# Optimization experiments

Hardware: AMD Instinct MI355X
Metric: run time of the kernel (lower is better)

The kernel has to match this reference:

```python
import jax, jax.numpy as jnp
import numpy as np

N, E, M, D = 100000, 50000, 1000000, 128  # vertices, hyperedges, incidences, hidden


def setup_inputs() -> dict:
    key = jax.random.key(0)
    ks = jax.random.split(key, 9)
    v = jax.random.normal(ks[0], (N, D), dtype=jnp.float32)
    e = jax.random.normal(ks[1], (E, D), dtype=jnp.float32)
    vidx = jax.random.randint(ks[2], (M,), 0, N)
    eidx = jax.random.randint(ks[3], (M,), 0, E)
    v_reg_weight = jax.random.uniform(ks[4], (M, 1), dtype=jnp.float32)
    e_reg_weight = jax.random.uniform(ks[5], (M, 1), dtype=jnp.float32)
    v_reg_sum = jnp.ones((N, 1), dtype=jnp.float32)
    e_reg_sum = jnp.ones((E, 1), dtype=jnp.float32)
    # learned parameters
    W_v2e = jax.random.normal(ks[6], (D, D), dtype=jnp.float32)
    W_e2v = jax.random.normal(ks[7], (D, D), dtype=jnp.float32)
    b_v = jnp.zeros((D,), dtype=jnp.float32)
    b_e = jnp.zeros((D,), dtype=jnp.float32)
    v_weight = jax.random.uniform(ks[8], (N, 1), dtype=jnp.float32)  # args.v_weight
    return dict(v=v, e=e, vidx=vidx, eidx=eidx,
                v_reg_weight=v_reg_weight, e_reg_weight=e_reg_weight,
                v_reg_sum=v_reg_sum, e_reg_sum=e_reg_sum,
                W_v2e=W_v2e, W_e2v=W_e2v, b_v=b_v, b_e=b_e, v_weight=v_weight)


def reference(v, e, vidx, eidx, v_reg_weight, e_reg_weight, v_reg_sum, e_reg_sum,
              W_v2e, W_e2v, b_v, b_e, v_weight):
    # v2e: dense transform, gather by vidx, reweight, scatter_add into edges
    ve = jax.nn.relu(v @ W_v2e + b_v)                      # [N, D]
    v_out = v * v_weight * 4.0                             # v_fac = 4
    msg_ve = (ve * v_weight)[vidx] * v_reg_weight          # [M, D]
    e_out = e + jax.ops.segment_sum(msg_ve, eidx, num_segments=E)
    e_out = e_out / e_reg_sum
    # e2v: dense transform, gather by eidx, reweight, scatter_add into vertices
    ev = jax.nn.relu(e_out @ W_e2v + b_e)                  # [E, D]
    msg_ev = (ev / 3.0)[eidx] * e_reg_weight               # [M, D]
    v_out = v_out + jax.ops.segment_sum(msg_ev, vidx, num_segments=N)
    v_out = v_out / v_reg_sum
    # is_last_mod=True: no dropout
    return v_out, e_out
```

## Files before the change

kernel.cpp:

```cpp
#include <hip/hip_runtime.h>
#include <cstddef>

#define DD 128
#define PART_ELEMS 4096
#define MAXB 256
#define MAXW 512
#define WT_LD 136

typedef __attribute__((ext_vector_type(8))) short bf16x8;
typedef __attribute__((ext_vector_type(4))) float f32x4;

__device__ __forceinline__ unsigned bf16pk(float x, float y) {
    unsigned a = __float_as_uint(x);
    unsigned b = __float_as_uint(y);
    a = (a + 0x7FFFu + ((a >> 16) & 1u)) >> 16;
    b = (b + 0x7FFFu + ((b >> 16) & 1u)) >> 16;
    return a | (b << 16);
}
__device__ __forceinline__ unsigned short bf16r(float x) {
    unsigned u = __float_as_uint(x);
    return (unsigned short)((u + 0x7FFFu + ((u >> 16) & 1u)) >> 16);
}
__device__ __forceinline__ float bflo(unsigned u) { return __uint_as_float(u << 16); }
__device__ __forceinline__ float bfhi(unsigned u) { return __uint_as_float(u & 0xFFFF0000u); }

__global__ __launch_bounds__(256)
void conv_w_kernel(const float* __restrict__ W0, const float* __restrict__ W1,
                   unsigned short* __restrict__ Wt0, unsigned short* __restrict__ Wt1,
                   int* __restrict__ bcur_e, int* __restrict__ bcur_v, int e_cap, int v_cap)
{
    int idx = blockIdx.x * 256 + threadIdx.x;
    int k = idx >> 7, c = idx & 127;
    Wt0[c * 128 + k] = bf16r(W0[idx]);
    Wt1[c * 128 + k] = bf16r(W1[idx]);
    if (blockIdx.x == 0) {
        bcur_e[threadIdx.x] = threadIdx.x * e_cap;
        bcur_v[threadIdx.x] = threadIdx.x * v_cap;
    }
}

__global__ __launch_bounds__(256)
void part2_kernel(const int* __restrict__ eidx, const int* __restrict__ vidx,
                  const float* __restrict__ vrw, const float* __restrict__ erw,
                  int* __restrict__ bcur_e, int* __restrict__ bcur_v,
                  int2* __restrict__ tmp_e, int2* __restrict__ tmp_v,
                  int M, int e_shift, int v_shift, int e_bk, int v_bk)
{
    __shared__ int lcnt_e[MAXB], lbase_e[MAXB], lcnt_v[MAXB], lbase_v[MAXB];
    const int t = threadIdx.x;
    const int base = blockIdx.x * PART_ELEMS;
    const int end = min(base + PART_ELEMS, M);

    if (t < e_bk) lcnt_e[t] = 0;
    if (t < v_bk) lcnt_v[t] = 0;
    __syncthreads();
    for (int j = base + t; j < end; j += 256) {
        atomicAdd(&lcnt_e[eidx[j] >> e_shift], 1);
        atomicAdd(&lcnt_v[vidx[j] >> v_shift], 1);
    }
    __syncthreads();
    if (t < e_bk) { int c = lcnt_e[t]; lbase_e[t] = c ? atomicAdd(&bcur_e[t], c) : 0; lcnt_e[t] = 0; }
    if (t < v_bk) { int c = lcnt_v[t]; lbase_v[t] = c ? atomicAdd(&bcur_v[t], c) : 0; lcnt_v[t] = 0; }
    __syncthreads();
    for (int j = base + t; j < end; j += 256) {
        int ei = eidx[j], vi = vidx[j];
        int wqe = (int)(vrw[j] * 32767.0f + 0.5f); wqe = wqe < 32767 ? wqe : 32767;
        int wqv = (int)(erw[j] * 32767.0f + 0.5f); wqv = wqv < 32767 ? wqv : 32767;
        int be = ei >> e_shift;
        int pe = lbase_e[be] + atomicAdd(&lcnt_e[be], 1);
        tmp_e[pe] = make_int2(ei | (wqe << 17), vi);
        int bv = vi >> v_shift;
        int pv = lbase_v[bv] + atomicAdd(&lcnt_v[bv], 1);
        tmp_v[pv] = make_int2(vi | (wqv << 17), ei);
    }
}

struct FineLds { int lcnt[MAXW]; int lstart[MAXW]; int sdata[256]; int scnt[256]; int spbase; };
struct GemmLds { unsigned short Wt[128 * WT_LD]; unsigned short At[64 * WT_LD]; };

__device__ __forceinline__
void fine_body(int blk, FineLds& L,
               const int2* __restrict__ tmp_e, const int* __restrict__ bcur_e,
               int e_cap, int e_shift, int En, int e_bk,
               int* __restrict__ e_start, unsigned* __restrict__ e_pack,
               const int2* __restrict__ tmp_v, const int* __restrict__ bcur_v,
               int v_cap, int v_shift, int Nn, int v_bk,
               int* __restrict__ v_start, unsigned* __restrict__ v_pack, int M)
{
    const int t = threadIdx.x;
    const int2* tmp; const int* bcur; int cap, shift, n, nb, b;
    int* start; unsigned* pack;
    if (blk < e_bk) {
        tmp = tmp_e; bcur = bcur_e; cap = e_cap; shift = e_shift; n = En; nb = e_bk;
        start = e_start; pack = e_pack; b = blk;
    } else {
        tmp = tmp_v; bcur = bcur_v; cap = v_cap; shift = v_shift; n = Nn; nb = v_bk;
        start = v_start; pack = v_pack; b = blk - e_bk;
    }

    int cnt_t = (t < nb) ? (bcur[t] - t * cap) : 0;
    L.scnt[t] = cnt_t;
    __syncthreads();
    int xx = cnt_t;
    for (int off = 1; off < 256; off <<= 1) {
        int y = (t >= off) ? L.scnt[t - off] : 0;
        __syncthreads();
        xx += y;
        L.scnt[t] = xx;
        __syncthreads();
    }
    if (t == b) L.spbase = xx - cnt_t;
    if (b == nb - 1 && t == 0) start[n] = M;
    __syncthreads();
    const int pbase = L.spbase;

    const int d0 = b << shift;
    const int width = min(1 << shift, n - d0);
    const int tbase = b * cap;
    const int nrec = bcur[b] - tbase;

    L.lcnt[t] = 0; L.lcnt[t + 256] = 0;
    __syncthreads();
    for (int j = t; j < nrec; j += 256)
        atomicAdd(&L.lcnt[(tmp[tbase + j].x & 0x1FFFF) - d0], 1);
    __syncthreads();
    int a = L.lcnt[2 * t], bb = L.lcnt[2 * t + 1];
    int s = a + bb;
    L.sdata[t] = s;
    __syncthreads();
    int x = s;
    for (int off = 1; off < 256; off <<= 1) {
        int y = (t >= off) ? L.sdata[t - off] : 0;
        __syncthreads();
        x += y;
        L.sdata[t] = x;
        __syncthreads();
    }
    int ex = x - s;
    L.lstart[2 * t] = ex;
    L.lstart[2 * t + 1] = ex + a;
    L.lcnt[2 * t] = 0; L.lcnt[2 * t + 1] = 0;
    __syncthreads();
    for (int i = t; i < width; i += 256)
        start[d0 + i] = pbase + L.lstart[i];
    for (int j = t; j < nrec; j += 256) {
        int2 r = tmp[tbase + j];
        int di = (r.x & 0x1FFFF) - d0;
        int pos = pbase + L.lstart[di] + atomicAdd(&L.lcnt[di], 1);
        pack[pos] = (unsigned)r.y | (((unsigned)r.x >> 17) << 17);
    }
}

__device__ __forceinline__
void gemm_body(int blk, GemmLds& L, const float* __restrict__ A,
               const unsigned short* __restrict__ Wtg, const float* __restrict__ bias,
               const float* __restrict__ rowwt, unsigned* __restrict__ outb,
               int nrows, float scale, bool v2e)
{
    const int t = threadIdx.x;
    const int row0 = blk * 64;

    {
        int r = t >> 1, h = t & 1;
        const uint4* src = reinterpret_cast<const uint4*>(Wtg + r * 128 + h * 64);
        uint4* dst = reinterpret_cast<uint4*>(&L.Wt[r * WT_LD + h * 64]);
        #pragma unroll
        for (int i = 0; i < 8; ++i) dst[i] = src[i];
    }
    {
        int r = t >> 2, q = t & 3;
        int grow = row0 + r;
        uint4 o[4];
        if (grow < nrows) {
            const float4* src = reinterpret_cast<const float4*>(A + (size_t)grow * DD + q * 32);
            #pragma unroll
            for (int i = 0; i < 4; ++i) {
                float4 f0 = src[2 * i];
                float4 f1 = src[2 * i + 1];
                o[i].x = bf16pk(f0.x, f0.y);
                o[i].y = bf16pk(f0.z, f0.w);
                o[i].z = bf16pk(f1.x, f1.y);
                o[i].w = bf16pk(f1.z, f1.w);
            }
        } else {
            #pragma unroll
            for (int i = 0; i < 4; ++i) o[i] = make_uint4(0, 0, 0, 0);
        }
        uint4* dst = reinterpret_cast<uint4*>(&L.At[r * WT_LD + q * 32]);
        #pragma unroll
        for (int i = 0; i < 4; ++i) dst[i] = o[i];
    }
    __syncthreads();

    const int w  = t >> 6;
    const int l  = t & 63;
    const int lr = l & 15;
    const int lk = (l >> 4) * 8;

    f32x4 acc[8];
    #pragma unroll
    for (int i = 0; i < 8; ++i) acc[i] = 0.0f;

    const int arow = w * 16 + lr;
    #pragma unroll
    for (int ks = 0; ks < 4; ++ks) {
        bf16x8 af = *reinterpret_cast<const bf16x8*>(&L.At[arow * WT_LD + lk + ks * 32]);
        #pragma unroll
        for (int ct = 0; ct < 8; ++ct) {
            bf16x8 bfr = *reinterpret_cast<const bf16x8*>(&L.Wt[(ct * 16 + lr) * WT_LD + lk + ks * 32]);
            acc[ct] = __builtin_amdgcn_mfma_f32_16x16x32_bf16(af, bfr, acc[ct], 0, 0, 0);
        }
    }

    float bcol[8];
    #pragma unroll
    for (int ct = 0; ct < 8; ++ct) bcol[ct] = bias[ct * 16 + lr];
    #pragma unroll
    for (int r = 0; r < 4; ++r) {
        int rl = w * 16 + (l >> 4) * 4 + r;
        int grow = row0 + rl;
        float rw = scale;
        if (v2e) rw = (grow < nrows) ? rowwt[grow] : 0.f;
        #pragma unroll
        for (int ct = 0; ct < 8; ++ct) {
            float val = fmaxf(acc[ct][r] + bcol[ct], 0.f) * rw;
            L.At[rl * WT_LD + ct * 16 + lr] = bf16r(val);
        }
    }
    {
        int r = t >> 2, part = t & 3;
        int grow = row0 + r;
        if (grow < nrows) {
            const uint4* src = reinterpret_cast<const uint4*>(&L.At[r * WT_LD + part * 32]);
            uint4* dst = reinterpret_cast<uint4*>(outb + (size_t)grow * 64 + part * 16);
            dst[0] = src[0]; dst[1] = src[1]; dst[2] = src[2]; dst[3] = src[3];
        }
    }
}

__global__ __launch_bounds__(256)
void fused_fine_gemm_kernel(const int2* __restrict__ tmp_e, const int* __restrict__ bcur_e,
                            int e_cap, int e_shift, int En, int e_bk,
                            int* __restrict__ e_start, unsigned* __restrict__ e_pack,
                            const int2* __restrict__ tmp_v, const int* __restrict__ bcur_v,
                            int v_cap, int v_shift, int Nn, int v_bk,
                            int* __restrict__ v_start, unsigned* __restrict__ v_pack, int M,
                            const float* __restrict__ v, const unsigned short* __restrict__ Wt0,
                            const float* __restrict__ bv, const float* __restrict__ vweight,
                            unsigned* __restrict__ vwb)
{
    __shared__ union SM { FineLds f; GemmLds g; } sm;
    const int nfine = e_bk + v_bk;
    if ((int)blockIdx.x < nfine) {
        fine_body(blockIdx.x, sm.f, tmp_e, bcur_e, e_cap, e_shift, En, e_bk, e_start, e_pack,
                  tmp_v, bcur_v, v_cap, v_shift, Nn, v_bk, v_start, v_pack, M);
    } else {
        gemm_body(blockIdx.x - nfine, sm.g, v, Wt0, bv, vweight, vwb, Nn, 1.0f, true);
    }
}

__global__ __launch_bounds__(256)
void gemm_mfma_kernel(const float* __restrict__ A, const unsigned short* __restrict__ Wtg,
                      const float* __restrict__ bias, unsigned* __restrict__ outb,
                      int nrows, float scale)
{
    __shared__ GemmLds sm;
    gemm_body(blockIdx.x, sm, A, Wtg, bias, nullptr, outb, nrows, scale, false);
}

__global__ __launch_bounds__(256)
void e_agg_kernel(const float* __restrict__ e, const unsigned* __restrict__ vwb,
                  const int* __restrict__ start, const unsigned* __restrict__ pack,
                  const float* __restrict__ ers, float* __restrict__ eout, int E)
{
    int row = blockIdx.x * 16 + (threadIdx.x >> 4);
    if (row >= E) return;
    int ql = threadIdx.x & 15;
    int s = start[row], t = start[row + 1];

    float a0=0.f,a1=0.f,a2=0.f,a3=0.f,a4=0.f,a5=0.f,a6=0.f,a7=0.f;
    float b0=0.f,b1=0.f,b2=0.f,b3=0.f,b4=0.f,b5=0.f,b6=0.f,b7=0.f;

    int j = s;
    for (; j + 2 <= t; j += 2) {
        unsigned pw0 = pack[j];
        unsigned pw1 = pack[j + 1];
        uint4 u0 = *reinterpret_cast<const uint4*>(&vwb[(size_t)(pw0 & 0x1FFFFu) * 64 + ql * 4]);
        uint4 u1 = *reinterpret_cast<const uint4*>(&vwb[(size_t)(pw1 & 0x1FFFFu) * 64 + ql * 4]);
        float w0 = (float)(pw0 >> 17) * (1.0f / 32767.0f);
        float w1 = (float)(pw1 >> 17) * (1.0f / 32767.0f);
        a0 = fmaf(bflo(u0.x), w0, a0); a1 = fmaf(bfhi(u0.x), w0, a1);
        a2 = fmaf(bflo(u0.y), w0, a2); a3 = fmaf(bfhi(u0.y), w0, a3);
        a4 = fmaf(bflo(u0.z), w0, a4); a5 = fmaf(bfhi(u0.z), w0, a5);
        a6 = fmaf(bflo(u0.w), w0, a6); a7 = fmaf(bfhi(u0.w), w0, a7);
        b0 = fmaf(bflo(u1.x), w1, b0); b1 = fmaf(bfhi(u1.x), w1, b1);
        b2 = fmaf(bflo(u1.y), w1, b2); b3 = fmaf(bfhi(u1.y), w1, b3);
        b4 = fmaf(bflo(u1.z), w1, b4); b5 = fmaf(bfhi(u1.z), w1, b5);
        b6 = fmaf(bflo(u1.w), w1, b6); b7 = fmaf(bfhi(u1.w), w1, b7);
    }
    if (j < t) {
        unsigned pw = pack[j];
        float wm = (float)(pw >> 17) * (1.0f / 32767.0f);
        uint4 u = *reinterpret_cast<const uint4*>(&vwb[(size_t)(pw & 0x1FFFFu) * 64 + ql * 4]);
        a0 = fmaf(bflo(u.x), wm, a0); a1 = fmaf(bfhi(u.x), wm, a1);
        a2 = fmaf(bflo(u.y), wm, a2); a3 = fmaf(bfhi(u.y), wm, a3);
        a4 = fmaf(bflo(u.z), wm, a4); a5 = fmaf(bfhi(u.z), wm, a5);
        a6 = fmaf(bflo(u.w), wm, a6); a7 = fmaf(bfhi(u.w), wm, a7);
    }
    float r0 = a0 + b0, r1 = a1 + b1, r2 = a2 + b2, r3 = a3 + b3;
    float r4 = a4 + b4, r5 = a5 + b5, r6 = a6 + b6, r7 = a7 + b7;

    float rs = 1.0f / ers[row];
    const float4* ep = reinterpret_cast<const float4*>(&e[(size_t)row * DD + ql * 8]);
    float4 e0 = ep[0], e1 = ep[1];
    float4 o0 = make_float4((e0.x + r0) * rs, (e0.y + r1) * rs, (e0.z + r2) * rs, (e0.w + r3) * rs);
    float4 o1 = make_float4((e1.x + r4) * rs, (e1.y + r5) * rs, (e1.z + r6) * rs, (e1.w + r7) * rs);
    float4* op = reinterpret_cast<float4*>(&eout[(size_t)row * DD + ql * 8]);
    op[0] = o0; op[1] = o1;
}

__global__ __launch_bounds__(256)
void v_agg_kernel(const float* __restrict__ v, const unsigned* __restrict__ evb,
                  const int* __restrict__ start, const unsigned* __restrict__ pack,
                  const float* __restrict__ vrs, const float* __restrict__ vweight,
                  float* __restrict__ vout, int N)
{
    int row = blockIdx.x * 16 + (threadIdx.x >> 4);
    if (row >= N) return;
    int ql = threadIdx.x & 15;
    int s = start[row], t = start[row + 1];

    float a0=0.f,a1=0.f,a2=0.f,a3=0.f,a4=0.f,a5=0.f,a6=0.f,a7=0.f;
    float b0=0.f,b1=0.f,b2=0.f,b3=0.f,b4=0.f,b5=0.f,b6=0.f,b7=0.f;

    int j = s;
    for (; j + 2 <= t; j += 2) {
        unsigned pw0 = pack[j];
        unsigned pw1 = pack[j + 1];
        uint4 u0 = *reinterpret_cast<const uint4*>(&evb[(size_t)(pw0 & 0x1FFFFu) * 64 + ql * 4]);
        uint4 u1 = *reinterpret_cast<const uint4*>(&evb[(size_t)(pw1 & 0x1FFFFu) * 64 + ql * 4]);
        float w0 = (float)(pw0 >> 17) * (1.0f / 32767.0f);
        float w1 = (float)(pw1 >> 17) * (1.0f / 32767.0f);
        a0 = fmaf(bflo(u0.x), w0, a0); a1 = fmaf(bfhi(u0.x), w0, a1);
        a2 = fmaf(bflo(u0.y), w0, a2); a3 = fmaf(bfhi(u0.y), w0, a3);
        a4 = fmaf(bflo(u0.z), w0, a4); a5 = fmaf(bfhi(u0.z), w0, a5);
        a6 = fmaf(bflo(u0.w), w0, a6); a7 = fmaf(bfhi(u0.w), w0, a7);
        b0 = fmaf(bflo(u1.x), w1, b0); b1 = fmaf(bfhi(u1.x), w1, b1);
        b2 = fmaf(bflo(u1.y), w1, b2); b3 = fmaf(bfhi(u1.y), w1, b3);
        b4 = fmaf(bflo(u1.z), w1, b4); b5 = fmaf(bfhi(u1.z), w1, b5);
        b6 = fmaf(bflo(u1.w), w1, b6); b7 = fmaf(bfhi(u1.w), w1, b7);
    }
    if (j < t) {
        unsigned pw = pack[j];
        float wm = (float)(pw >> 17) * (1.0f / 32767.0f);
        uint4 u = *reinterpret_cast<const uint4*>(&evb[(size_t)(pw & 0x1FFFFu) * 64 + ql * 4]);
        a0 = fmaf(bflo(u.x), wm, a0); a1 = fmaf(bfhi(u.x), wm, a1);
        a2 = fmaf(bflo(u.y), wm, a2); a3 = fmaf(bfhi(u.y), wm, a3);
        a4 = fmaf(bflo(u.z), wm, a4); a5 = fmaf(bfhi(u.z), wm, a5);
        a6 = fmaf(bflo(u.w), wm, a6); a7 = fmaf(bfhi(u.w), wm, a7);
    }
    float r0 = a0 + b0, r1 = a1 + b1, r2 = a2 + b2, r3 = a3 + b3;
    float r4 = a4 + b4, r5 = a5 + b5, r6 = a6 + b6, r7 = a7 + b7;

    float rs = 1.0f / vrs[row];
    float wt = vweight[row] * 4.0f;
    const float4* vp = reinterpret_cast<const float4*>(&v[(size_t)row * DD + ql * 8]);
    float4 v0 = vp[0], v1 = vp[1];
    float4 o0 = make_float4((v0.x * wt + r0) * rs, (v0.y * wt + r1) * rs,
                            (v0.z * wt + r2) * rs, (v0.w * wt + r3) * rs);
    float4 o1 = make_float4((v1.x * wt + r4) * rs, (v1.y * wt + r5) * rs,
                            (v1.z * wt + r6) * rs, (v1.w * wt + r7) * rs);
    float4* op = reinterpret_cast<float4*>(&vout[(size_t)row * DD + ql * 8]);
    op[0] = o0; op[1] = o1;
}

extern "C" void kernel_launch(void* const* d_in, const int* in_sizes, int n_in,
                              void* d_out, int out_size, void* d_ws, size_t ws_size,
                              hipStream_t stream)
{
    const float* v       = (const float*)d_in[0];
    const float* e       = (const float*)d_in[1];
    const int*   vidx    = (const int*)d_in[2];
    const int*   eidx    = (const int*)d_in[3];
    const float* vrw     = (const float*)d_in[4];
    const float* erw     = (const float*)d_in[5];
    const float* vrs     = (const float*)d_in[6];
    const float* ers     = (const float*)d_in[7];
    const float* Wv2e    = (const float*)d_in[8];
    const float* We2v    = (const float*)d_in[9];
    const float* bv      = (const float*)d_in[10];
    const float* be      = (const float*)d_in[11];
    const float* vweight = (const float*)d_in[12];

    const int N = in_sizes[0] / DD;
    const int E = in_sizes[1] / DD;
    const int M = in_sizes[2];

    float* vout = (float*)d_out;
    float* eout = vout + (size_t)N * DD;

    auto calc_shift = [](int n) {
        int s = 0;
        while (((n + (1 << s) - 1) >> s) > MAXB) ++s;
        return s;
    };
    const int e_shift = calc_shift(E);
    const int v_shift = calc_shift(N);
    const int e_bk = (E + (1 << e_shift) - 1) >> e_shift;
    const int v_bk = (N + (1 << v_shift) - 1) >> v_shift;
    const int e_cap = ((M / e_bk) * 3) / 2 + 256;
    const int v_cap = ((M / v_bk) * 3) / 2 + 256;

    char* wsb = (char*)d_ws;
    size_t off = 0;
    auto alloc = [&](size_t bytes) { char* p = wsb + off; off += (bytes + 255) & ~(size_t)255; return p; };
    unsigned* vwb   = (unsigned*)alloc((size_t)N * 64 * sizeof(unsigned));
    unsigned* evb   = vwb;
    int*   e_start = (int*)alloc((size_t)(E + 1) * sizeof(int));
    int*   v_start = (int*)alloc((size_t)(N + 1) * sizeof(int));
    int*   bcur_e  = (int*)alloc(MAXB * sizeof(int));
    int*   bcur_v  = (int*)alloc(MAXB * sizeof(int));
    unsigned short* Wt0 = (unsigned short*)alloc(DD * DD * sizeof(unsigned short));
    unsigned short* Wt1 = (unsigned short*)alloc(DD * DD * sizeof(unsigned short));
    unsigned* e_pack = (unsigned*)alloc((size_t)M * sizeof(unsigned));
    unsigned* v_pack = (unsigned*)alloc((size_t)M * sizeof(unsigned));
    int2*  tmp_e   = (int2*)alloc((size_t)e_bk * e_cap * sizeof(int2));
    int2*  tmp_v   = (int2*)alloc((size_t)v_bk * v_cap * sizeof(int2));

    const int pblk = (M + PART_ELEMS - 1) / PART_ELEMS;
    const int gblkN = (N + 63) / 64;

    conv_w_kernel<<<64, 256, 0, stream>>>(Wv2e, We2v, Wt0, Wt1, bcur_e, bcur_v, e_cap, v_cap);
    part2_kernel<<<pblk, 256, 0, stream>>>(eidx, vidx, vrw, erw, bcur_e, bcur_v,
                                           tmp_e, tmp_v, M, e_shift, v_shift, e_bk, v_bk);
    fused_fine_gemm_kernel<<<e_bk + v_bk + gblkN, 256, 0, stream>>>(
        tmp_e, bcur_e, e_cap, e_shift, E, e_bk, e_start, e_pack,
        tmp_v, bcur_v, v_cap, v_shift, N, v_bk, v_start, v_pack, M,
        v, Wt0, bv, vweight, vwb);
    e_agg_kernel<<<(E + 15) / 16, 256, 0, stream>>>(e, vwb, e_start, e_pack, ers, eout, E);
    gemm_mfma_kernel<<<(E + 63) / 64, 256, 0, stream>>>(eout, Wt1, be, evb, E, 1.0f / 3.0f);
    v_agg_kernel<<<(N + 15) / 16, 256, 0, stream>>>(v, evb, v_start, v_pack, vrs, vweight, vout, N);
}
```

Measured before the change: 187.8 us.

## Fuse edge aggregation with e2v GEMM and read weights from global memory

The edge aggregation and the e2v MFMA GEMM are merged into one kernel. Each block aggregates 64 edge rows, writes eout, packs the rows to bf16 in LDS and runs the GEMM on them directly, so eout is no longer read back from global memory and one launch is removed. The weight tile is no longer staged in LDS; B fragments are read from global memory (likely L2-resident), which cuts LDS use but adds uncoalesced global reads. Bucket cursors are now zeroed with memsets and the per-bucket offsets are applied in the partition kernel, and evb gets its own buffer instead of aliasing vwb.

```diff
diff --git a/kernel.cpp b/kernel.cpp
--- a/kernel.cpp
+++ b/kernel.cpp
@@ -26,17 +26,12 @@
 
 __global__ __launch_bounds__(256)
 void conv_w_kernel(const float* __restrict__ W0, const float* __restrict__ W1,
-                   unsigned short* __restrict__ Wt0, unsigned short* __restrict__ Wt1,
-                   int* __restrict__ bcur_e, int* __restrict__ bcur_v, int e_cap, int v_cap)
+                   unsigned short* __restrict__ Wt0, unsigned short* __restrict__ Wt1)
 {
     int idx = blockIdx.x * 256 + threadIdx.x;
     int k = idx >> 7, c = idx & 127;
     Wt0[c * 128 + k] = bf16r(W0[idx]);
     Wt1[c * 128 + k] = bf16r(W1[idx]);
-    if (blockIdx.x == 0) {
-        bcur_e[threadIdx.x] = threadIdx.x * e_cap;
-        bcur_v[threadIdx.x] = threadIdx.x * v_cap;
-    }
 }
 
 __global__ __launch_bounds__(256)
@@ -44,7 +39,8 @@
                   const float* __restrict__ vrw, const float* __restrict__ erw,
                   int* __restrict__ bcur_e, int* __restrict__ bcur_v,
                   int2* __restrict__ tmp_e, int2* __restrict__ tmp_v,
-                  int M, int e_shift, int v_shift, int e_bk, int v_bk)
+                  int M, int e_shift, int v_shift, int e_bk, int v_bk,
+                  int e_cap, int v_cap)
 {
     __shared__ int lcnt_e[MAXB], lbase_e[MAXB], lcnt_v[MAXB], lbase_v[MAXB];
     const int t = threadIdx.x;
@@ -59,8 +55,8 @@
         atomicAdd(&lcnt_v[vidx[j] >> v_shift], 1);
     }
     __syncthreads();
-    if (t < e_bk) { int c = lcnt_e[t]; lbase_e[t] = c ? atomicAdd(&bcur_e[t], c) : 0; lcnt_e[t] = 0; }
-    if (t < v_bk) { int c = lcnt_v[t]; lbase_v[t] = c ? atomicAdd(&bcur_v[t], c) : 0; lcnt_v[t] = 0; }
+    if (t < e_bk) { int c = lcnt_e[t]; lbase_e[t] = t * e_cap + (c ? atomicAdd(&bcur_e[t], c) : 0); lcnt_e[t] = 0; }
+    if (t < v_bk) { int c = lcnt_v[t]; lbase_v[t] = t * v_cap + (c ? atomicAdd(&bcur_v[t], c) : 0); lcnt_v[t] = 0; }
     __syncthreads();
     for (int j = base + t; j < end; j += 256) {
         int ei = eidx[j], vi = vidx[j];
@@ -76,7 +72,7 @@
 }
 
 struct FineLds { int lcnt[MAXW]; int lstart[MAXW]; int sdata[256]; int scnt[256]; int spbase; };
-struct GemmLds { unsigned short Wt[128 * WT_LD]; unsigned short At[64 * WT_LD]; };
+struct GemmLds { unsigned short At[64 * WT_LD]; };
 
 __device__ __forceinline__
 void fine_body(int blk, FineLds& L,
@@ -98,7 +94,7 @@
         start = v_start; pack = v_pack; b = blk - e_bk;
     }
 
-    int cnt_t = (t < nb) ? (bcur[t] - t * cap) : 0;
+    int cnt_t = (t < nb) ? bcur[t] : 0;
     L.scnt[t] = cnt_t;
     __syncthreads();
     int xx = cnt_t;
@@ -117,7 +113,7 @@
     const int d0 = b << shift;
     const int width = min(1 << shift, n - d0);
     const int tbase = b * cap;
-    const int nrec = bcur[b] - tbase;
+    const int nrec = bcur[b];
 
     L.lcnt[t] = 0; L.lcnt[t + 256] = 0;
     __syncthreads();
@@ -152,21 +148,13 @@
 }
 
 __device__ __forceinline__
-void gemm_body(int blk, GemmLds& L, const float* __restrict__ A,
-               const unsigned short* __restrict__ Wtg, const float* __restrict__ bias,
-               const float* __restrict__ rowwt, unsigned* __restrict__ outb,
-               int nrows, float scale, bool v2e)
+void gemm_body_v2e(int blk, GemmLds& L, const float* __restrict__ A,
+                   const unsigned short* __restrict__ Wtg, const float* __restrict__ bias,
+                   const float* __restrict__ rowwt, unsigned* __restrict__ outb, int nrows)
 {
     const int t = threadIdx.x;
     const int row0 = blk * 64;
 
-    {
-        int r = t >> 1, h = t & 1;
-        const uint4* src = reinterpret_cast<const uint4*>(Wtg + r * 128 + h * 64);
-        uint4* dst = reinterpret_cast<uint4*>(&L.Wt[r * WT_LD + h * 64]);
-        #pragma unroll
-        for (int i = 0; i < 8; ++i) dst[i] = src[i];
-    }
     {
         int r = t >> 2, q = t & 3;
         int grow = row0 + r;
@@ -207,7 +195,7 @@
         bf16x8 af = *reinterpret_cast<const bf16x8*>(&L.At[arow * WT_LD + lk + ks * 32]);
         #pragma unroll
         for (int ct = 0; ct < 8; ++ct) {
-            bf16x8 bfr = *reinterpret_cast<const bf16x8*>(&L.Wt[(ct * 16 + lr) * WT_LD + lk + ks * 32]);
+            bf16x8 bfr = *reinterpret_cast<const bf16x8*>(&Wtg[(ct * 16 + lr) * 128 + lk + ks * 32]);
             acc[ct] = __builtin_amdgcn_mfma_f32_16x16x32_bf16(af, bfr, acc[ct], 0, 0, 0);
         }
     }
@@ -219,8 +207,7 @@
     for (int r = 0; r < 4; ++r) {
         int rl = w * 16 + (l >> 4) * 4 + r;
         int grow = row0 + rl;
-        float rw = scale;
-        if (v2e) rw = (grow < nrows) ? rowwt[grow] : 0.f;
+        float rw = (grow < nrows) ? rowwt[grow] : 0.f;
         #pragma unroll
         for (int ct = 0; ct < 8; ++ct) {
             float val = fmaxf(acc[ct][r] + bcol[ct], 0.f) * rw;
@@ -255,68 +242,117 @@
         fine_body(blockIdx.x, sm.f, tmp_e, bcur_e, e_cap, e_shift, En, e_bk, e_start, e_pack,
                   tmp_v, bcur_v, v_cap, v_shift, Nn, v_bk, v_start, v_pack, M);
     } else {
-        gemm_body(blockIdx.x - nfine, sm.g, v, Wt0, bv, vweight, vwb, Nn, 1.0f, true);
+        gemm_body_v2e(blockIdx.x - nfine, sm.g, v, Wt0, bv, vweight, vwb, Nn);
     }
 }
 
 __global__ __launch_bounds__(256)
-void gemm_mfma_kernel(const float* __restrict__ A, const unsigned short* __restrict__ Wtg,
-                      const float* __restrict__ bias, unsigned* __restrict__ outb,
-                      int nrows, float scale)
-{
-    __shared__ GemmLds sm;
-    gemm_body(blockIdx.x, sm, A, Wtg, bias, nullptr, outb, nrows, scale, false);
-}
-
-__global__ __launch_bounds__(256)
-void e_agg_kernel(const float* __restrict__ e, const unsigned* __restrict__ vwb,
-                  const int* __restrict__ start, const unsigned* __restrict__ pack,
-                  const float* __restrict__ ers, float* __restrict__ eout, int E)
-{
-    int row = blockIdx.x * 16 + (threadIdx.x >> 4);
-    if (row >= E) return;
-    int ql = threadIdx.x & 15;
-    int s = start[row], t = start[row + 1];
-
-    float a0=0.f,a1=0.f,a2=0.f,a3=0.f,a4=0.f,a5=0.f,a6=0.f,a7=0.f;
-    float b0=0.f,b1=0.f,b2=0.f,b3=0.f,b4=0.f,b5=0.f,b6=0.f,b7=0.f;
-
-    int j = s;
-    for (; j + 2 <= t; j += 2) {
-        unsigned pw0 = pack[j];
-        unsigned pw1 = pack[j + 1];
-        uint4 u0 = *reinterpret_cast<const uint4*>(&vwb[(size_t)(pw0 & 0x1FFFFu) * 64 + ql * 4]);
-        uint4 u1 = *reinterpret_cast<const uint4*>(&vwb[(size_t)(pw1 & 0x1FFFFu) * 64 + ql * 4]);
-        float w0 = (float)(pw0 >> 17) * (1.0f / 32767.0f);
-        float w1 = (float)(pw1 >> 17) * (1.0f / 32767.0f);
-        a0 = fmaf(bflo(u0.x), w0, a0); a1 = fmaf(bfhi(u0.x), w0, a1);
-        a2 = fmaf(bflo(u0.y), w0, a2); a3 = fmaf(bfhi(u0.y), w0, a3);
-        a4 = fmaf(bflo(u0.z), w0, a4); a5 = fmaf(bfhi(u0.z), w0, a5);
-        a6 = fmaf(bflo(u0.w), w0, a6); a7 = fmaf(bfhi(u0.w), w0, a7);
-        b0 = fmaf(bflo(u1.x), w1, b0); b1 = fmaf(bfhi(u1.x), w1, b1);
-        b2 = fmaf(bflo(u1.y), w1, b2); b3 = fmaf(bfhi(u1.y), w1, b3);
-        b4 = fmaf(bflo(u1.z), w1, b4); b5 = fmaf(bfhi(u1.z), w1, b5);
-        b6 = fmaf(bflo(u1.w), w1, b6); b7 = fmaf(bfhi(u1.w), w1, b7);
-    }
-    if (j < t) {
-        unsigned pw = pack[j];
-        float wm = (float)(pw >> 17) * (1.0f / 32767.0f);
-        uint4 u = *reinterpret_cast<const uint4*>(&vwb[(size_t)(pw & 0x1FFFFu) * 64 + ql * 4]);
-        a0 = fmaf(bflo(u.x), wm, a0); a1 = fmaf(bfhi(u.x), wm, a1);
-        a2 = fmaf(bflo(u.y), wm, a2); a3 = fmaf(bfhi(u.y), wm, a3);
-        a4 = fmaf(bflo(u.z), wm, a4); a5 = fmaf(bfhi(u.z), wm, a5);
-        a6 = fmaf(bflo(u.w), wm, a6); a7 = fmaf(bfhi(u.w), wm, a7);
-    }
-    float r0 = a0 + b0, r1 = a1 + b1, r2 = a2 + b2, r3 = a3 + b3;
-    float r4 = a4 + b4, r5 = a5 + b5, r6 = a6 + b6, r7 = a7 + b7;
-
-    float rs = 1.0f / ers[row];
-    const float4* ep = reinterpret_cast<const float4*>(&e[(size_t)row * DD + ql * 8]);
-    float4 e0 = ep[0], e1 = ep[1];
-    float4 o0 = make_float4((e0.x + r0) * rs, (e0.y + r1) * rs, (e0.z + r2) * rs, (e0.w + r3) * rs);
-    float4 o1 = make_float4((e1.x + r4) * rs, (e1.y + r5) * rs, (e1.z + r6) * rs, (e1.w + r7) * rs);
-    float4* op = reinterpret_cast<float4*>(&eout[(size_t)row * DD + ql * 8]);
-    op[0] = o0; op[1] = o1;
+void agg_gemm_kernel(const float* __restrict__ e, const unsigned* __restrict__ vwb,
+                     const int* __restrict__ start, const unsigned* __restrict__ pack,
+                     const float* __restrict__ ers, float* __restrict__ eout,
+                     const unsigned short* __restrict__ Wtg, const float* __restrict__ be,
+                     unsigned* __restrict__ evb, int E)
+{
+    __shared__ unsigned short At[64 * WT_LD];
+    const int t = threadIdx.x;
+    const int row0 = blockIdx.x * 64;
+    const int g = t >> 4, ql = t & 15;
+
+    #pragma unroll
+    for (int rr = 0; rr < 4; ++rr) {
+        int rl = g + rr * 16;
+        int row = row0 + rl;
+        uint4 pkd = make_uint4(0, 0, 0, 0);
+        if (row < E) {
+            int s = start[row], tt = start[row + 1];
+            float a0=0.f,a1=0.f,a2=0.f,a3=0.f,a4=0.f,a5=0.f,a6=0.f,a7=0.f;
+            float b0=0.f,b1=0.f,b2=0.f,b3=0.f,b4=0.f,b5=0.f,b6=0.f,b7=0.f;
+            int j = s;
+            for (; j + 2 <= tt; j += 2) {
+                unsigned pw0 = pack[j];
+                unsigned pw1 = pack[j + 1];
+                uint4 u0 = *reinterpret_cast<const uint4*>(&vwb[(size_t)(pw0 & 0x1FFFFu) * 64 + ql * 4]);
+                uint4 u1 = *reinterpret_cast<const uint4*>(&vwb[(size_t)(pw1 & 0x1FFFFu) * 64 + ql * 4]);
+                float w0 = (float)(pw0 >> 17) * (1.0f / 32767.0f);
+                float w1 = (float)(pw1 >> 17) * (1.0f / 32767.0f);
+                a0 = fmaf(bflo(u0.x), w0, a0); a1 = fmaf(bfhi(u0.x), w0, a1);
+                a2 = fmaf(bflo(u0.y), w0, a2); a3 = fmaf(bfhi(u0.y), w0, a3);
+                a4 = fmaf(bflo(u0.z), w0, a4); a5 = fmaf(bfhi(u0.z), w0, a5);
+                a6 = fmaf(bflo(u0.w), w0, a6); a7 = fmaf(bfhi(u0.w), w0, a7);
+                b0 = fmaf(bflo(u1.x), w1, b0); b1 = fmaf(bfhi(u1.x), w1, b1);
+                b2 = fmaf(bflo(u1.y), w1, b2); b3 = fmaf(bfhi(u1.y), w1, b3);
+                b4 = fmaf(bflo(u1.z), w1, b4); b5 = fmaf(bfhi(u1.z), w1, b5);
+                b6 = fmaf(bflo(u1.w), w1, b6); b7 = fmaf(bfhi(u1.w), w1, b7);
+            }
+            if (j < tt) {
+                unsigned pw = pack[j];
+                float wm = (float)(pw >> 17) * (1.0f / 32767.0f);
+                uint4 u = *reinterpret_cast<const uint4*>(&vwb[(size_t)(pw & 0x1FFFFu) * 64 + ql * 4]);
+                a0 = fmaf(bflo(u.x), wm, a0); a1 = fmaf(bfhi(u.x), wm, a1);
+                a2 = fmaf(bflo(u.y), wm, a2); a3 = fmaf(bfhi(u.y), wm, a3);
+                a4 = fmaf(bflo(u.z), wm, a4); a5 = fmaf(bfhi(u.z), wm, a5);
+                a6 = fmaf(bflo(u.w), wm, a6); a7 = fmaf(bfhi(u.w), wm, a7);
+            }
+            float r0 = a0 + b0, r1 = a1 + b1, r2 = a2 + b2, r3 = a3 + b3;
+            float r4 = a4 + b4, r5 = a5 + b5, r6 = a6 + b6, r7 = a7 + b7;
+            float rs = 1.0f / ers[row];
+            const float4* ep = reinterpret_cast<const float4*>(&e[(size_t)row * DD + ql * 8]);
+            float4 e0 = ep[0], e1 = ep[1];
+            float4 o0 = make_float4((e0.x + r0) * rs, (e0.y + r1) * rs, (e0.z + r2) * rs, (e0.w + r3) * rs);
+            float4 o1 = make_float4((e1.x + r4) * rs, (e1.y + r5) * rs, (e1.z + r6) * rs, (e1.w + r7) * rs);
+            float4* op = reinterpret_cast<float4*>(&eout[(size_t)row * DD + ql * 8]);
+            op[0] = o0; op[1] = o1;
+            pkd.x = bf16pk(o0.x, o0.y);
+            pkd.y = bf16pk(o0.z, o0.w);
+            pkd.z = bf16pk(o1.x, o1.y);
+            pkd.w = bf16pk(o1.z, o1.w);
+        }
+        *reinterpret_cast<uint4*>(&At[rl * WT_LD + ql * 8]) = pkd;
+    }
+    __syncthreads();
+
+    const int w  = t >> 6;
+    const int l  = t & 63;
+    const int lr = l & 15;
+    const int lk = (l >> 4) * 8;
+
+    f32x4 acc[8];
+    #pragma unroll
+    for (int i = 0; i < 8; ++i) acc[i] = 0.0f;
+
+    const int arow = w * 16 + lr;
+    #pragma unroll
+    for (int ks = 0; ks < 4; ++ks) {
+        bf16x8 af = *reinterpret_cast<const bf16x8*>(&At[arow * WT_LD + lk + ks * 32]);
+        #pragma unroll
+        for (int ct = 0; ct < 8; ++ct) {
+            bf16x8 bfr = *reinterpret_cast<const bf16x8*>(&Wtg[(ct * 16 + lr) * 128 + lk + ks * 32]);
+            acc[ct] = __builtin_amdgcn_mfma_f32_16x16x32_bf16(af, bfr, acc[ct], 0, 0, 0);
+        }
+    }
+
+    float bcol[8];
+    #pragma unroll
+    for (int ct = 0; ct < 8; ++ct) bcol[ct] = be[ct * 16 + lr];
+    const float third = 1.0f / 3.0f;
+    #pragma unroll
+    for (int r = 0; r < 4; ++r) {
+        int rl = w * 16 + (l >> 4) * 4 + r;
+        #pragma unroll
+        for (int ct = 0; ct < 8; ++ct) {
+            float val = fmaxf(acc[ct][r] + bcol[ct], 0.f) * third;
+            At[rl * WT_LD + ct * 16 + lr] = bf16r(val);
+        }
+    }
+    {
+        int r = t >> 2, part = t & 3;
+        int grow = row0 + r;
+        if (grow < E) {
+            const uint4* src = reinterpret_cast<const uint4*>(&At[r * WT_LD + part * 32]);
+            uint4* dst = reinterpret_cast<uint4*>(evb + (size_t)grow * 64 + part * 16);
+            dst[0] = src[0]; dst[1] = src[1]; dst[2] = src[2]; dst[3] = src[3];
+        }
+    }
 }
 
 __global__ __launch_bounds__(256)
@@ -415,7 +451,7 @@
     size_t off = 0;
     auto alloc = [&](size_t bytes) { char* p = wsb + off; off += (bytes + 255) & ~(size_t)255; return p; };
     unsigned* vwb   = (unsigned*)alloc((size_t)N * 64 * sizeof(unsigned));
-    unsigned* evb   = vwb;
+    unsigned* evb   = (unsigned*)alloc((size_t)E * 64 * sizeof(unsigned));
     int*   e_start = (int*)alloc((size_t)(E + 1) * sizeof(int));
     int*   v_start = (int*)alloc((size_t)(N + 1) * sizeof(int));
     int*   bcur_e  = (int*)alloc(MAXB * sizeof(int));
@@ -430,14 +466,17 @@
     const int pblk = (M + PART_ELEMS - 1) / PART_ELEMS;
     const int gblkN = (N + 63) / 64;
 
-    conv_w_kernel<<<64, 256, 0, stream>>>(Wv2e, We2v, Wt0, Wt1, bcur_e, bcur_v, e_cap, v_cap);
+    hipMemsetAsync(bcur_e, 0, MAXB * sizeof(int), stream);
+    hipMemsetAsync(bcur_v, 0, MAXB * sizeof(int), stream);
+    conv_w_kernel<<<64, 256, 0, stream>>>(Wv2e, We2v, Wt0, Wt1);
     part2_kernel<<<pblk, 256, 0, stream>>>(eidx, vidx, vrw, erw, bcur_e, bcur_v,
-                                           tmp_e, tmp_v, M, e_shift, v_shift, e_bk, v_bk);
+                                           tmp_e, tmp_v, M, e_shift, v_shift, e_bk, v_bk,
+                                           e_cap, v_cap);
     fused_fine_gemm_kernel<<<e_bk + v_bk + gblkN, 256, 0, stream>>>(
         tmp_e, bcur_e, e_cap, e_shift, E, e_bk, e_start, e_pack,
         tmp_v, bcur_v, v_cap, v_shift, N, v_bk, v_start, v_pack, M,
         v, Wt0, bv, vweight, vwb);
-    e_agg_kernel<<<(E + 15) / 16, 256, 0, stream>>>(e, vwb, e_start, e_pack, ers, eout, E);
-    gemm_mfma_kernel<<<(E + 63) / 64, 256, 0, stream>>>(eout, Wt1, be, evb, E, 1.0f / 3.0f);
+    agg_gemm_kernel<<<(E + 63) / 64, 256, 0, stream>>>(e, vwb, e_start, e_pack, ers, eout,
+                                                       Wt1, be, evb, E);
     v_agg_kernel<<<(N + 15) / 16, 256, 0, stream>>>(v, evb, v_start, v_pack, vrs, vweight, vout, N);
 }
```

Measured after the change: 201.6 us. 1.07x slower.
